# Performance work log

Hardware: AMD Instinct MI355X
Metric: run time of the kernel (lower is better)

## Reference

```python
import jax, jax.numpy as jnp
import numpy as np


def setup_inputs() -> dict:
    key = jax.random.key(0)
    k1, k2 = jax.random.split(key)
    latents = jax.random.normal(k1, (8, 8192, 256), dtype=jnp.float32)
    weights = jax.random.normal(k2, (1024, 256), dtype=jnp.float32)
    return {"latents": latents, "weights": weights}


def reference(latents, weights):
    # Nearest-codebook search. Torch materializes [B,N,K,D] sub then takes
    # the L2 norm; argmin over the norm equals argmin over squared distance,
    x2 = jnp.sum(latents * latents, axis=-1, keepdims=True)          # [B,N,1]
    w2 = jnp.sum(weights * weights, axis=-1)                         # [K]
    xw = jnp.einsum('bnd,kd->bnk', latents, weights)                 # [B,N,K]
    dist2 = x2 - 2.0 * xw + w2                                       # [B,N,K]
    encoding_inds = jnp.argmin(dist2, axis=-1)                       # [B,N]
    quantized = weights[encoding_inds]                               # [B,N,D]

    # codebook / commitment losses are computed in the original but then
    # the result is overwritten; reproduce the final (used) loss only.
    dot_loss = jnp.sum(latents * quantized, axis=-1)                 # [B,N]
    vq_loss = jnp.sum(jax.nn.softmax(dot_loss, axis=-1))             # scalar

    # straight-through estimator
    quantized_st = latents + jax.lax.stop_gradient(quantized - latents)
    return quantized_st, vq_loss
```

## Files before the change

### kernel.cpp

```cpp
#include <hip/hip_runtime.h>
#include <cstddef>

#define DD     256
#define NCODES 1024
#define MTOT   65536
#define MB     128
#define WSTR   264

typedef __attribute__((ext_vector_type(8))) short short8v;
typedef __attribute__((ext_vector_type(4))) float f32x4;

__device__ __forceinline__ float xla_seq_fma_sumsq256(const float* __restrict__ a) {
    float acc = 0.f;
    #pragma unroll 8
    for (int d = 0; d < 256; ++d)
        acc = __builtin_fmaf(a[d], a[d], acc);
    return acc;
}

__device__ __forceinline__ float chain_fma_dot256(const float* __restrict__ x,
                                                  const float* __restrict__ w) {
    float acc = 0.f;
    #pragma unroll 8
    for (int d = 0; d < 256; ++d)
        acc = __builtin_fmaf(x[d], w[d], acc);
    return acc;
}

__device__ __forceinline__ short bf16_rne(float f) {
    unsigned u = __builtin_bit_cast(unsigned, f);
    u = u + 0x7FFFu + ((u >> 16) & 1u);
    return (short)(u >> 16);
}

__global__ __launch_bounds__(256) void w2_kernel(const float* __restrict__ W,
                                                 float* __restrict__ w2) {
    int c = blockIdx.x * 256 + threadIdx.x;
    if (c >= NCODES) return;
    w2[c] = xla_seq_fma_sumsq256(W + (size_t)c * DD);
}

__global__ __launch_bounds__(256) void wprep_kernel(const float* __restrict__ W,
                                                    short* __restrict__ Wbf) {
    const int t = blockIdx.x * 256 + threadIdx.x;
    const float4 v = *reinterpret_cast<const float4*>(W + (size_t)t * 4);
    short4 s;
    s.x = bf16_rne(v.x); s.y = bf16_rne(v.y);
    s.z = bf16_rne(v.z); s.w = bf16_rne(v.w);
    *reinterpret_cast<short4*>(Wbf + (size_t)t * 4) = s;
}

#define DECL3(S) \
    float v0_##S = 3.4e38f, v1_##S = 3.4e38f, v2_##S = 3.4e38f; \
    int   i0_##S = 0,       i1_##S = 0,       i2_##S = 0

#define INS3T(S, NV, NI) do {                                            \
    const float _nv = (NV); const int _ni = (NI);                        \
    if (_nv < v0_##S)      { v2_##S = v1_##S; i2_##S = i1_##S;           \
                             v1_##S = v0_##S; i1_##S = i0_##S;           \
                             v0_##S = _nv;    i0_##S = _ni; }            \
    else if (_nv < v1_##S) { v2_##S = v1_##S; i2_##S = i1_##S;           \
                             v1_##S = _nv;    i1_##S = _ni; }            \
    else if (_nv < v2_##S) { v2_##S = _nv;    i2_##S = _ni; }            \
} while (0)

#define MERGE3T(S, M) do {                                               \
    const float _o0 = __shfl_xor(v0_##S, (M));                           \
    const int   _q0 = __shfl_xor(i0_##S, (M));                           \
    const float _o1 = __shfl_xor(v1_##S, (M));                           \
    const int   _q1 = __shfl_xor(i1_##S, (M));                           \
    const float _o2 = __shfl_xor(v2_##S, (M));                           \
    const int   _q2 = __shfl_xor(i2_##S, (M));                           \
    INS3T(S, _o0, _q0);                                                  \
    INS3T(S, _o1, _q1);                                                  \
    INS3T(S, _o2, _q2);                                                  \
} while (0)

#define WRITE3T(S, R) do {                                               \
    int _a = i0_##S, _b = i1_##S, _c = i2_##S, _t;                       \
    if (_a > _b) { _t = _a; _a = _b; _b = _t; }                          \
    if (_b > _c) { _t = _b; _b = _c; _c = _t; }                          \
    if (_a > _b) { _t = _a; _a = _b; _b = _t; }                          \
    cand[R][0] = _a; cand[R][1] = _b; cand[R][2] = _c;                   \
} while (0)

__global__ __launch_bounds__(256, 2) void vq_main(
    const float* __restrict__ X, const short* __restrict__ Wbf,
    const float* __restrict__ W, const float* __restrict__ w2g,
    float* __restrict__ out, float* __restrict__ dl)
{
    __shared__ short Wl[64 * WSTR];
    __shared__ float w2s[NCODES];
    __shared__ int   cand[MB][3];
    __shared__ int   idx_s[MB];
    __shared__ float rr_x2[MB];
    __shared__ float rr_xw[MB][3];

    const int tid  = threadIdx.x;
    const int lane = tid & 63;
    const int wv   = tid >> 6;
    const int m0   = blockIdx.x * MB;
    const int lg   = lane & 15;
    const int kb   = (lane >> 4) * 8;

    for (int i = tid; i < NCODES; i += 256) w2s[i] = w2g[i];

    const int arowA = m0 + wv * 32 + lg;
    const int arowB = arowA + 16;
    short8v aA[8], aB[8];
    #pragma unroll
    for (int kg = 0; kg < 8; ++kg) {
        const float* srcA = X + (size_t)arowA * DD + kg * 32 + kb;
        const float4 xa0 = *reinterpret_cast<const float4*>(srcA);
        const float4 xa1 = *reinterpret_cast<const float4*>(srcA + 4);
        short8v sa;
        sa[0] = bf16_rne(xa0.x); sa[1] = bf16_rne(xa0.y);
        sa[2] = bf16_rne(xa0.z); sa[3] = bf16_rne(xa0.w);
        sa[4] = bf16_rne(xa1.x); sa[5] = bf16_rne(xa1.y);
        sa[6] = bf16_rne(xa1.z); sa[7] = bf16_rne(xa1.w);
        aA[kg] = sa;
        const float* srcB = X + (size_t)arowB * DD + kg * 32 + kb;
        const float4 xb0 = *reinterpret_cast<const float4*>(srcB);
        const float4 xb1 = *reinterpret_cast<const float4*>(srcB + 4);
        short8v sb;
        sb[0] = bf16_rne(xb0.x); sb[1] = bf16_rne(xb0.y);
        sb[2] = bf16_rne(xb0.z); sb[3] = bf16_rne(xb0.w);
        sb[4] = bf16_rne(xb1.x); sb[5] = bf16_rne(xb1.y);
        sb[6] = bf16_rne(xb1.z); sb[7] = bf16_rne(xb1.w);
        aB[kg] = sb;
    }

    DECL3(A0); DECL3(A1); DECL3(A2); DECL3(A3);
    DECL3(B0); DECL3(B1); DECL3(B2); DECL3(B3);

    for (int ct = 0; ct < NCODES / 64; ++ct) {
        const int c0 = ct * 64;
        __syncthreads();
        #pragma unroll
        for (int l = 0; l < 8; ++l) {
            const int f    = tid + l * 256;
            const int code = f >> 5;
            const int ch   = f & 31;
            const uint4 wv4 = *reinterpret_cast<const uint4*>(
                Wbf + (size_t)(c0 + code) * DD + ch * 8);
            *reinterpret_cast<uint4*>(&Wl[code * WSTR + ch * 8]) = wv4;
        }
        __syncthreads();

        f32x4 accA0 = {0.f,0.f,0.f,0.f}, accA1 = {0.f,0.f,0.f,0.f};
        f32x4 accA2 = {0.f,0.f,0.f,0.f}, accA3 = {0.f,0.f,0.f,0.f};
        f32x4 accB0 = {0.f,0.f,0.f,0.f}, accB1 = {0.f,0.f,0.f,0.f};
        f32x4 accB2 = {0.f,0.f,0.f,0.f}, accB3 = {0.f,0.f,0.f,0.f};

        #pragma unroll
        for (int kg = 0; kg < 8; ++kg) {
            const short8v b0 = *reinterpret_cast<const short8v*>(
                &Wl[(0 * 16 + lg) * WSTR + kg * 32 + kb]);
            const short8v b1 = *reinterpret_cast<const short8v*>(
                &Wl[(1 * 16 + lg) * WSTR + kg * 32 + kb]);
            const short8v b2 = *reinterpret_cast<const short8v*>(
                &Wl[(2 * 16 + lg) * WSTR + kg * 32 + kb]);
            const short8v b3 = *reinterpret_cast<const short8v*>(
                &Wl[(3 * 16 + lg) * WSTR + kg * 32 + kb]);
            accA0 = __builtin_amdgcn_mfma_f32_16x16x32_bf16(aA[kg], b0, accA0, 0, 0, 0);
            accB0 = __builtin_amdgcn_mfma_f32_16x16x32_bf16(aB[kg], b0, accB0, 0, 0, 0);
            accA1 = __builtin_amdgcn_mfma_f32_16x16x32_bf16(aA[kg], b1, accA1, 0, 0, 0);
            accB1 = __builtin_amdgcn_mfma_f32_16x16x32_bf16(aB[kg], b1, accB1, 0, 0, 0);
            accA2 = __builtin_amdgcn_mfma_f32_16x16x32_bf16(aA[kg], b2, accA2, 0, 0, 0);
            accB2 = __builtin_amdgcn_mfma_f32_16x16x32_bf16(aB[kg], b2, accB2, 0, 0, 0);
            accA3 = __builtin_amdgcn_mfma_f32_16x16x32_bf16(aA[kg], b3, accA3, 0, 0, 0);
            accB3 = __builtin_amdgcn_mfma_f32_16x16x32_bf16(aB[kg], b3, accB3, 0, 0, 0);
        }

        {
            const int   c   = c0 + 0 * 16 + lg;
            const float w2v = w2s[c];
            INS3T(A0, __builtin_fmaf(-2.f, accA0[0], w2v), c);
            INS3T(A1, __builtin_fmaf(-2.f, accA0[1], w2v), c);
            INS3T(A2, __builtin_fmaf(-2.f, accA0[2], w2v), c);
            INS3T(A3, __builtin_fmaf(-2.f, accA0[3], w2v), c);
            INS3T(B0, __builtin_fmaf(-2.f, accB0[0], w2v), c);
            INS3T(B1, __builtin_fmaf(-2.f, accB0[1], w2v), c);
            INS3T(B2, __builtin_fmaf(-2.f, accB0[2], w2v), c);
            INS3T(B3, __builtin_fmaf(-2.f, accB0[3], w2v), c);
        }
        {
            const int   c   = c0 + 1 * 16 + lg;
            const float w2v = w2s[c];
            INS3T(A0, __builtin_fmaf(-2.f, accA1[0], w2v), c);
            INS3T(A1, __builtin_fmaf(-2.f, accA1[1], w2v), c);
            INS3T(A2, __builtin_fmaf(-2.f, accA1[2], w2v), c);
            INS3T(A3, __builtin_fmaf(-2.f, accA1[3], w2v), c);
            INS3T(B0, __builtin_fmaf(-2.f, accB1[0], w2v), c);
            INS3T(B1, __builtin_fmaf(-2.f, accB1[1], w2v), c);
            INS3T(B2, __builtin_fmaf(-2.f, accB1[2], w2v), c);
            INS3T(B3, __builtin_fmaf(-2.f, accB1[3], w2v), c);
        }
        {
            const int   c   = c0 + 2 * 16 + lg;
            const float w2v = w2s[c];
            INS3T(A0, __builtin_fmaf(-2.f, accA2[0], w2v), c);
            INS3T(A1, __builtin_fmaf(-2.f, accA2[1], w2v), c);
            INS3T(A2, __builtin_fmaf(-2.f, accA2[2], w2v), c);
            INS3T(A3, __builtin_fmaf(-2.f, accA2[3], w2v), c);
            INS3T(B0, __builtin_fmaf(-2.f, accB2[0], w2v), c);
            INS3T(B1, __builtin_fmaf(-2.f, accB2[1], w2v), c);
            INS3T(B2, __builtin_fmaf(-2.f, accB2[2], w2v), c);
            INS3T(B3, __builtin_fmaf(-2.f, accB2[3], w2v), c);
        }
        {
            const int   c   = c0 + 3 * 16 + lg;
            const float w2v = w2s[c];
            INS3T(A0, __builtin_fmaf(-2.f, accA3[0], w2v), c);
            INS3T(A1, __builtin_fmaf(-2.f, accA3[1], w2v), c);
            INS3T(A2, __builtin_fmaf(-2.f, accA3[2], w2v), c);
            INS3T(A3, __builtin_fmaf(-2.f, accA3[3], w2v), c);
            INS3T(B0, __builtin_fmaf(-2.f, accB3[0], w2v), c);
            INS3T(B1, __builtin_fmaf(-2.f, accB3[1], w2v), c);
            INS3T(B2, __builtin_fmaf(-2.f, accB3[2], w2v), c);
            INS3T(B3, __builtin_fmaf(-2.f, accB3[3], w2v), c);
        }
    }

    #pragma unroll
    for (int m = 1; m <= 8; m <<= 1) {
        MERGE3T(A0, m); MERGE3T(A1, m); MERGE3T(A2, m); MERGE3T(A3, m);
        MERGE3T(B0, m); MERGE3T(B1, m); MERGE3T(B2, m); MERGE3T(B3, m);
    }
    if (lg == 0) {
        const int rbA = wv * 32 + (lane >> 4) * 4;
        WRITE3T(A0, rbA + 0);  WRITE3T(A1, rbA + 1);
        WRITE3T(A2, rbA + 2);  WRITE3T(A3, rbA + 3);
        WRITE3T(B0, rbA + 16); WRITE3T(B1, rbA + 17);
        WRITE3T(B2, rbA + 18); WRITE3T(B3, rbA + 19);
    }
    __syncthreads();

    {
        const int r = tid >> 1;
        const int u = tid & 1;
        const float* xr = X + (size_t)(m0 + r) * DD;
        if (u == 0) {
            rr_x2[r]    = xla_seq_fma_sumsq256(xr);
            rr_xw[r][0] = chain_fma_dot256(xr, W + (size_t)cand[r][0] * DD);
        } else {
            rr_xw[r][1] = chain_fma_dot256(xr, W + (size_t)cand[r][1] * DD);
            rr_xw[r][2] = chain_fma_dot256(xr, W + (size_t)cand[r][2] * DD);
        }
    }
    __syncthreads();

    if (tid < MB) {
#pragma clang fp contract(off)
        const int b0 = cand[tid][0], b1 = cand[tid][1], b2 = cand[tid][2];
        const float x2  = rr_x2[tid];
        const float xw0 = rr_xw[tid][0];
        const float xw1 = rr_xw[tid][1];
        const float xw2 = rr_xw[tid][2];
        const float dd0 = (x2 - 2.0f * xw0) + w2s[b0];
        const float dd1 = (x2 - 2.0f * xw1) + w2s[b1];
        const float dd2 = (x2 - 2.0f * xw2) + w2s[b2];
        int pick = b0; float best = dd0; float pd = xw0;
        if (dd1 < best) { best = dd1; pick = b1; pd = xw1; }
        if (dd2 < best) { best = dd2; pick = b2; pd = xw2; }
        idx_s[tid] = pick;
        dl[m0 + tid] = pd;
    }
    __syncthreads();

    const float4* W4 = reinterpret_cast<const float4*>(W);
    float4*       O4 = reinterpret_cast<float4*>(out);
    #pragma unroll
    for (int l = 0; l < 32; ++l) {
        const int e  = tid + l * 256;
        const int r  = e >> 6;
        const int c4 = e & 63;
        O4[(size_t)(m0 + r) * (DD / 4) + c4] =
            W4[(size_t)idx_s[r] * (DD / 4) + c4];
    }
}

__global__ __launch_bounds__(256) void vq_loss_partial(const float* __restrict__ dl,
                                                       float* __restrict__ partial) {
    __shared__ float red[256];
    const int tid = threadIdx.x;
    const int b   = blockIdx.x;
    const float* row = dl + (size_t)b * 8192;

    float lm = -3.4e38f;
    for (int i = tid; i < 8192; i += 256) lm = fmaxf(lm, row[i]);
    red[tid] = lm; __syncthreads();
    for (int s = 128; s > 0; s >>= 1) {
        if (tid < s) red[tid] = fmaxf(red[tid], red[tid + s]);
        __syncthreads();
    }
    const float mx = red[0]; __syncthreads();

    float ls = 0.f;
    for (int i = tid; i < 8192; i += 256) ls += expf(row[i] - mx);
    red[tid] = ls; __syncthreads();
    for (int s = 128; s > 0; s >>= 1) {
        if (tid < s) red[tid] += red[tid + s];
        __syncthreads();
    }
    const float Z = red[0]; __syncthreads();

    float lc = 0.f;
    for (int i = tid; i < 8192; i += 256) lc += expf(row[i] - mx) / Z;
    red[tid] = lc; __syncthreads();
    for (int s = 128; s > 0; s >>= 1) {
        if (tid < s) red[tid] += red[tid + s];
        __syncthreads();
    }
    if (tid == 0) partial[b] = red[0];
}

__global__ void vq_loss_final(const float* __restrict__ partial,
                              float* __restrict__ outv) {
    if (threadIdx.x == 0) {
        float t = 0.f;
        for (int b = 0; b < 8; ++b) t += partial[b];
        outv[0] = t;
    }
}

extern "C" void kernel_launch(void* const* d_in, const int* in_sizes, int n_in,
                              void* d_out, int out_size, void* d_ws, size_t ws_size,
                              hipStream_t stream) {
    const float* X = (const float*)d_in[0];
    const float* W = (const float*)d_in[1];
    float* out = (float*)d_out;
    float* w2      = (float*)d_ws;
    float* dlv     = w2 + NCODES;
    float* partial = dlv + MTOT;
    short* Wbf     = (short*)(partial + 8);

    w2_kernel      <<<NCODES / 256,            256, 0, stream>>>(W, w2);
    wprep_kernel   <<<NCODES * DD / 4 / 256,   256, 0, stream>>>(W, Wbf);
    vq_main        <<<MTOT / MB,               256, 0, stream>>>(X, Wbf, W, w2, out, dlv);
    vq_loss_partial<<<8,                       256, 0, stream>>>(dlv, partial);
    vq_loss_final  <<<1,                        64, 0, stream>>>(partial, out + (size_t)MTOT * DD);
}
```

Before: 184.3 us.

## Double-buffer codebook tiles in LDS and merge w2 into bf16 prep kernel

The main kernel now keeps two LDS buffers for codebook tiles. It issues global loads for the next 64-code tile into registers before the MFMA and top-3 work on the current tile, then stores them to the other buffer afterwards, so each iteration needs one barrier instead of two. The separate w2 norm kernel is folded into the bf16 conversion kernel to save a launch. The cost is double the Wl LDS footprint (about 33KB to 67KB) and extra live registers for the prefetched data, which could cut the occupancy target of two blocks per CU.

```diff
diff --git a/kernel.cpp b/kernel.cpp
--- a/kernel.cpp
+++ b/kernel.cpp
@@ -33,21 +33,19 @@
     return (short)(u >> 16);
 }
 
-__global__ __launch_bounds__(256) void w2_kernel(const float* __restrict__ W,
-                                                 float* __restrict__ w2) {
-    int c = blockIdx.x * 256 + threadIdx.x;
-    if (c >= NCODES) return;
-    w2[c] = xla_seq_fma_sumsq256(W + (size_t)c * DD);
-}
-
-__global__ __launch_bounds__(256) void wprep_kernel(const float* __restrict__ W,
-                                                    short* __restrict__ Wbf) {
+__global__ __launch_bounds__(256) void wprep_w2_kernel(const float* __restrict__ W,
+                                                       short* __restrict__ Wbf,
+                                                       float* __restrict__ w2) {
     const int t = blockIdx.x * 256 + threadIdx.x;
     const float4 v = *reinterpret_cast<const float4*>(W + (size_t)t * 4);
     short4 s;
     s.x = bf16_rne(v.x); s.y = bf16_rne(v.y);
     s.z = bf16_rne(v.z); s.w = bf16_rne(v.w);
     *reinterpret_cast<short4*>(Wbf + (size_t)t * 4) = s;
+    if (threadIdx.x < 4) {
+        const int c = blockIdx.x * 4 + threadIdx.x;
+        w2[c] = xla_seq_fma_sumsq256(W + (size_t)c * DD);
+    }
 }
 
 #define DECL3(S) \
@@ -89,7 +87,7 @@
     const float* __restrict__ W, const float* __restrict__ w2g,
     float* __restrict__ out, float* __restrict__ dl)
 {
-    __shared__ short Wl[64 * WSTR];
+    __shared__ short Wl[2][64 * WSTR];
     __shared__ float w2s[NCODES];
     __shared__ int   cand[MB][3];
     __shared__ int   idx_s[MB];
@@ -104,6 +102,31 @@
     const int kb   = (lane >> 4) * 8;
 
     for (int i = tid; i < NCODES; i += 256) w2s[i] = w2g[i];
+
+    const int code0 = (tid +   0) >> 5, ch0 = (tid +   0) & 31;
+    const int code1 = (tid + 256) >> 5, ch1 = (tid + 256) & 31;
+    const int code2 = (tid + 512) >> 5, ch2 = (tid + 512) & 31;
+    const int code3 = (tid + 768) >> 5, ch3 = (tid + 768) & 31;
+    const int code4 = (tid +1024) >> 5, ch4 = (tid +1024) & 31;
+    const int code5 = (tid +1280) >> 5, ch5 = (tid +1280) & 31;
+    const int code6 = (tid +1536) >> 5, ch6 = (tid +1536) & 31;
+    const int code7 = (tid +1792) >> 5, ch7 = (tid +1792) & 31;
+    const size_t so0 = (size_t)code0 * DD + ch0 * 8;
+    const size_t so1 = (size_t)code1 * DD + ch1 * 8;
+    const size_t so2 = (size_t)code2 * DD + ch2 * 8;
+    const size_t so3 = (size_t)code3 * DD + ch3 * 8;
+    const size_t so4 = (size_t)code4 * DD + ch4 * 8;
+    const size_t so5 = (size_t)code5 * DD + ch5 * 8;
+    const size_t so6 = (size_t)code6 * DD + ch6 * 8;
+    const size_t so7 = (size_t)code7 * DD + ch7 * 8;
+    const int do0 = code0 * WSTR + ch0 * 8;
+    const int do1 = code1 * WSTR + ch1 * 8;
+    const int do2 = code2 * WSTR + ch2 * 8;
+    const int do3 = code3 * WSTR + ch3 * 8;
+    const int do4 = code4 * WSTR + ch4 * 8;
+    const int do5 = code5 * WSTR + ch5 * 8;
+    const int do6 = code6 * WSTR + ch6 * 8;
+    const int do7 = code7 * WSTR + ch7 * 8;
 
     const int arowA = m0 + wv * 32 + lg;
     const int arowB = arowA + 16;
@@ -133,19 +156,46 @@
     DECL3(A0); DECL3(A1); DECL3(A2); DECL3(A3);
     DECL3(B0); DECL3(B1); DECL3(B2); DECL3(B3);
 
+    {
+        const short* base = Wbf;
+        const uint4 p0 = *reinterpret_cast<const uint4*>(base + so0);
+        const uint4 p1 = *reinterpret_cast<const uint4*>(base + so1);
+        const uint4 p2 = *reinterpret_cast<const uint4*>(base + so2);
+        const uint4 p3 = *reinterpret_cast<const uint4*>(base + so3);
+        const uint4 p4 = *reinterpret_cast<const uint4*>(base + so4);
+        const uint4 p5 = *reinterpret_cast<const uint4*>(base + so5);
+        const uint4 p6 = *reinterpret_cast<const uint4*>(base + so6);
+        const uint4 p7 = *reinterpret_cast<const uint4*>(base + so7);
+        *reinterpret_cast<uint4*>(&Wl[0][do0]) = p0;
+        *reinterpret_cast<uint4*>(&Wl[0][do1]) = p1;
+        *reinterpret_cast<uint4*>(&Wl[0][do2]) = p2;
+        *reinterpret_cast<uint4*>(&Wl[0][do3]) = p3;
+        *reinterpret_cast<uint4*>(&Wl[0][do4]) = p4;
+        *reinterpret_cast<uint4*>(&Wl[0][do5]) = p5;
+        *reinterpret_cast<uint4*>(&Wl[0][do6]) = p6;
+        *reinterpret_cast<uint4*>(&Wl[0][do7]) = p7;
+    }
+    __syncthreads();
+
     for (int ct = 0; ct < NCODES / 64; ++ct) {
-        const int c0 = ct * 64;
-        __syncthreads();
-        #pragma unroll
-        for (int l = 0; l < 8; ++l) {
-            const int f    = tid + l * 256;
-            const int code = f >> 5;
-            const int ch   = f & 31;
-            const uint4 wv4 = *reinterpret_cast<const uint4*>(
-                Wbf + (size_t)(c0 + code) * DD + ch * 8);
-            *reinterpret_cast<uint4*>(&Wl[code * WSTR + ch * 8]) = wv4;
-        }
-        __syncthreads();
+        const int cur = ct & 1;
+        const int c0  = ct * 64;
+        const bool pfv = (ct < NCODES / 64 - 1);
+
+        uint4 p0, p1, p2, p3, p4, p5, p6, p7;
+        if (pfv) {
+            const short* base = Wbf + (size_t)(c0 + 64) * DD;
+            p0 = *reinterpret_cast<const uint4*>(base + so0);
+            p1 = *reinterpret_cast<const uint4*>(base + so1);
+            p2 = *reinterpret_cast<const uint4*>(base + so2);
+            p3 = *reinterpret_cast<const uint4*>(base + so3);
+            p4 = *reinterpret_cast<const uint4*>(base + so4);
+            p5 = *reinterpret_cast<const uint4*>(base + so5);
+            p6 = *reinterpret_cast<const uint4*>(base + so6);
+            p7 = *reinterpret_cast<const uint4*>(base + so7);
+        }
+
+        const short* wl = Wl[cur];
 
         f32x4 accA0 = {0.f,0.f,0.f,0.f}, accA1 = {0.f,0.f,0.f,0.f};
         f32x4 accA2 = {0.f,0.f,0.f,0.f}, accA3 = {0.f,0.f,0.f,0.f};
@@ -155,13 +205,13 @@
         #pragma unroll
         for (int kg = 0; kg < 8; ++kg) {
             const short8v b0 = *reinterpret_cast<const short8v*>(
-                &Wl[(0 * 16 + lg) * WSTR + kg * 32 + kb]);
+                &wl[(0 * 16 + lg) * WSTR + kg * 32 + kb]);
             const short8v b1 = *reinterpret_cast<const short8v*>(
-                &Wl[(1 * 16 + lg) * WSTR + kg * 32 + kb]);
+                &wl[(1 * 16 + lg) * WSTR + kg * 32 + kb]);
             const short8v b2 = *reinterpret_cast<const short8v*>(
-                &Wl[(2 * 16 + lg) * WSTR + kg * 32 + kb]);
+                &wl[(2 * 16 + lg) * WSTR + kg * 32 + kb]);
             const short8v b3 = *reinterpret_cast<const short8v*>(
-                &Wl[(3 * 16 + lg) * WSTR + kg * 32 + kb]);
+                &wl[(3 * 16 + lg) * WSTR + kg * 32 + kb]);
             accA0 = __builtin_amdgcn_mfma_f32_16x16x32_bf16(aA[kg], b0, accA0, 0, 0, 0);
             accB0 = __builtin_amdgcn_mfma_f32_16x16x32_bf16(aB[kg], b0, accB0, 0, 0, 0);
             accA1 = __builtin_amdgcn_mfma_f32_16x16x32_bf16(aA[kg], b1, accA1, 0, 0, 0);
@@ -220,6 +270,19 @@
             INS3T(B2, __builtin_fmaf(-2.f, accB3[2], w2v), c);
             INS3T(B3, __builtin_fmaf(-2.f, accB3[3], w2v), c);
         }
+
+        if (pfv) {
+            short* wn = Wl[cur ^ 1];
+            *reinterpret_cast<uint4*>(&wn[do0]) = p0;
+            *reinterpret_cast<uint4*>(&wn[do1]) = p1;
+            *reinterpret_cast<uint4*>(&wn[do2]) = p2;
+            *reinterpret_cast<uint4*>(&wn[do3]) = p3;
+            *reinterpret_cast<uint4*>(&wn[do4]) = p4;
+            *reinterpret_cast<uint4*>(&wn[do5]) = p5;
+            *reinterpret_cast<uint4*>(&wn[do6]) = p6;
+            *reinterpret_cast<uint4*>(&wn[do7]) = p7;
+        }
+        __syncthreads();
     }
 
     #pragma unroll
@@ -335,9 +398,8 @@
     float* partial = dlv + MTOT;
     short* Wbf     = (short*)(partial + 8);
 
-    w2_kernel      <<<NCODES / 256,            256, 0, stream>>>(W, w2);
-    wprep_kernel   <<<NCODES * DD / 4 / 256,   256, 0, stream>>>(W, Wbf);
-    vq_main        <<<MTOT / MB,               256, 0, stream>>>(X, Wbf, W, w2, out, dlv);
-    vq_loss_partial<<<8,                       256, 0, stream>>>(dlv, partial);
-    vq_loss_final  <<<1,                        64, 0, stream>>>(partial, out + (size_t)MTOT * DD);
-}
+    wprep_w2_kernel<<<NCODES * DD / 4 / 256, 256, 0, stream>>>(W, Wbf, w2);
+    vq_main        <<<MTOT / MB,             256, 0, stream>>>(X, Wbf, W, w2, out, dlv);
+    vq_loss_partial<<<8,                     256, 0, stream>>>(dlv, partial);
+    vq_loss_final  <<<1,                      64, 0, stream>>>(partial, out + (size_t)MTOT * DD);
+}
```

Result: faster. 168.1 us (-8.8%).
